# Kernel tuning notes

Hardware: AMD Instinct MI355X
Metric: run time of the kernel (lower is better)

## Reference

```python
import jax, jax.numpy as jnp
import numpy as np

N_EMBED = 384
NUM_HEADS = 6
HEAD_SIZE = 64
B, T = 128, 256


def setup_inputs() -> dict:
    key = jax.random.key(0)
    ks = jax.random.split(key, 6)
    x = jax.random.normal(ks[0], (B, T, N_EMBED), dtype=jnp.float32)
    s = 0.02
    Wq = jax.random.normal(ks[1], (NUM_HEADS, N_EMBED, HEAD_SIZE), dtype=jnp.float32) * s
    Wk = jax.random.normal(ks[2], (NUM_HEADS, N_EMBED, HEAD_SIZE), dtype=jnp.float32) * s
    Wv = jax.random.normal(ks[3], (NUM_HEADS, N_EMBED, HEAD_SIZE), dtype=jnp.float32) * s
    Wp = jax.random.normal(ks[4], (NUM_HEADS * HEAD_SIZE, N_EMBED), dtype=jnp.float32) * s
    bp = jnp.zeros((N_EMBED,), dtype=jnp.float32)
    return {"x": x, "Wq": Wq, "Wk": Wk, "Wv": Wv, "Wp": Wp, "bp": bp}


def reference(x, Wq, Wk, Wv, Wp, bp):
    # x: [B,T,C]; Wq/Wk/Wv: [H,C,hs]; Wp: [H*hs, C]
    Bx, Tx, C = x.shape
    q = jnp.einsum('btc,hcd->bhtd', x, Wq)
    k = jnp.einsum('btc,hcd->bhtd', x, Wk)
    v = jnp.einsum('btc,hcd->bhtd', x, Wv)
    scale = HEAD_SIZE ** (-0.5)
    scores = jnp.einsum('bhtd,bhsd->bhts', q, k) * scale  # [B,H,T,T]
    causal = jnp.tril(jnp.ones((Tx, Tx), dtype=bool))
    scores = jnp.where(causal, scores, -jnp.inf)
    attn = jax.nn.softmax(scores, axis=-1)
    # dropout is identity in eval mode
    out = jnp.einsum('bhts,bhsd->bhtd', attn, v)  # [B,H,T,hs]
    out = out.transpose(0, 2, 1, 3).reshape(Bx, Tx, NUM_HEADS * HEAD_SIZE)
    return out @ Wp + bp
```

## Files before the change

kernel.cpp:

```cpp
#include <hip/hip_runtime.h>
#include <hip/hip_bf16.h>

#define C_DIM 384
#define H_NUM 6
#define HS    64
#define B_DIM 128
#define T_DIM 256
#define NROWS (B_DIM * T_DIM)

typedef unsigned short u16;
typedef unsigned int u32;
typedef short bf16x8 __attribute__((ext_vector_type(8)));
typedef float floatx4 __attribute__((ext_vector_type(4)));

__device__ __forceinline__ u16 f2b(float f) {
  __hip_bfloat16 h = __float2bfloat16(f);
  u16 u;
  __builtin_memcpy(&u, &h, 2);
  return u;
}
__device__ __forceinline__ void gload_lds16(const void* g, void* lds) {
  __builtin_amdgcn_global_load_lds(
      (const __attribute__((address_space(1))) u32*)g,
      (__attribute__((address_space(3))) u32*)lds, 16, 0, 0);
}

__global__ __launch_bounds__(256) void prep_kernel(
    const float* __restrict__ x, const float* __restrict__ Wq,
    const float* __restrict__ Wk, const float* __restrict__ Wv,
    const float* __restrict__ Wp, u16* __restrict__ xb,
    u16* __restrict__ Wh, u16* __restrict__ Wpt) {
  const int bid = blockIdx.x;
  const int tid = threadIdx.x;
  if (bid < 6144) {
    const int i = bid * 256 + tid;
    const int row = (i * 8) / C_DIM;
    const int c8 = (i * 8) % C_DIM;
    const int cs = c8 ^ ((row & 7) << 3);
    const float* p = x + (size_t)row * C_DIM + cs;
    const float4 f0 = *(const float4*)p;
    const float4 f1 = *(const float4*)(p + 4);
    bf16x8 pk;
    pk[0] = (short)f2b(f0.x); pk[1] = (short)f2b(f0.y);
    pk[2] = (short)f2b(f0.z); pk[3] = (short)f2b(f0.w);
    pk[4] = (short)f2b(f1.x); pk[5] = (short)f2b(f1.y);
    pk[6] = (short)f2b(f1.z); pk[7] = (short)f2b(f1.w);
    ((bf16x8*)xb)[i] = pk;
  } else {
    const int idx = (bid - 6144) * 256 + tid;
    const int WHN = H_NUM * 192 * C_DIM;
    if (idx < WHN) {
      int h = idx / (192 * C_DIM);
      int rem = idx % (192 * C_DIM);
      int r = rem / C_DIM, c = rem % C_DIM;
      int tz = r >> 6, d = r & 63;
      const int cs = c ^ ((r & 7) << 3);
      const float* W = (tz == 0) ? Wq : (tz == 1) ? Wk : Wv;
      Wh[idx] = f2b(W[((size_t)h * C_DIM + cs) * HS + d]);
    } else {
      int j = idx - WHN;
      int n = j / C_DIM, c = j % C_DIM;
      const int cs = c ^ ((n & 7) << 3);
      Wpt[j] = f2b(Wp[cs * C_DIM + n]);
    }
  }
}

#define AS0_OFF 0
#define AS1_OFF 16384
#define BS0_OFF 32768
#define BS1_OFF 45056
#define QS_OFF  0
#define KLS_OFF 16384
#define VTS_OFF 32768
#define PLS_OFF 49152

template <bool DIAG>
__device__ __forceinline__ void attn_chunk_f(int c, int mt, int lane, int ln,
                                             int qd, const bf16x8* qf,
                                             const u16* smem, u16* Pw,
                                             floatx4* oacc, float* lsum) {
  floatx4 sacc[4];
#pragma unroll
  for (int st = 0; st < 4; ++st) {
    sacc[st] = floatx4{0.f, 0.f, 0.f, 0.f};
#pragma unroll
    for (int kc = 0; kc < 2; ++kc) {
      bf16x8 kf = *(const bf16x8*)&smem[KLS_OFF + ((c * 4 + st) * 2 + kc) * 512 +
                                        lane * 8];
      sacc[st] =
          __builtin_amdgcn_mfma_f32_16x16x32_bf16(qf[kc], kf, sacc[st], 0, 0, 0);
    }
  }
#pragma unroll
  for (int st = 0; st < 4; ++st) {
#pragma unroll
    for (int r = 0; r < 4; ++r) {
      const float sv = sacc[st][r] * 0.125f;
      float p = __expf(sv);
      if (DIAG) {
        const bool ok = (c * 64 + st * 16 + ln) <= (mt * 16 + qd * 4 + r);
        p = ok ? p : 0.f;
      }
      lsum[r] += p;
      Pw[(qd * 4 + r) * 72 + st * 16 + ln] = f2b(p);
    }
  }
#pragma unroll
  for (int kc2 = 0; kc2 < 2; ++kc2) {
    bf16x8 pf = *(const bf16x8*)&Pw[ln * 72 + kc2 * 32 + qd * 8];
#pragma unroll
    for (int dt = 0; dt < 4; ++dt) {
      bf16x8 vf = *(const bf16x8*)&smem[VTS_OFF + (dt * 16 + ln) * 256 +
                                        ((c * 64 + kc2 * 32 + qd * 8) ^
                                         ((ln & 7) << 3))];
      oacc[dt] =
          __builtin_amdgcn_mfma_f32_16x16x32_bf16(pf, vf, oacc[dt], 0, 0, 0);
    }
  }
}

__global__ __launch_bounds__(512) void qkv_attn_fused(
    const u16* __restrict__ xb, const u16* __restrict__ Wh,
    u16* __restrict__ y) {
  __shared__ __align__(16) u16 smem[58368];
  const int b = blockIdx.x;
  const int h = blockIdx.y;
  const u16* a_rows = xb + (size_t)b * 256 * C_DIM;
  const u16* wbase = Wh + (size_t)h * 192 * C_DIM;

  const int tid = threadIdx.x;
  const int lane = tid & 63;
  const int w = tid >> 6;
  const int lr = lane >> 3;
  const int lkc = (lane & 7) * 8;
  const int qd = lane >> 4;
  const int ln = lane & 15;
  const int sx = (ln & 7) << 3;
  const int wm = (w >> 1) * 64;
  const int wn = (w & 1) * 96;

  floatx4 acc[4][6];
#pragma unroll
  for (int i = 0; i < 4; ++i)
#pragma unroll
    for (int j = 0; j < 6; ++j) acc[i][j] = floatx4{0.f, 0.f, 0.f, 0.f};

#pragma unroll
  for (int s = 0; s < 4; ++s) {
    const int rbase = (s * 8 + w) * 8;
    gload_lds16(a_rows + (size_t)(rbase + lr) * C_DIM + lkc,
                smem + AS0_OFF + rbase * 64);
  }
#pragma unroll
  for (int s = 0; s < 3; ++s) {
    const int rbase = (s * 8 + w) * 8;
    gload_lds16(wbase + (size_t)(rbase + lr) * C_DIM + lkc,
                smem + BS0_OFF + rbase * 64);
  }

  for (int kb = 0; kb < 6; ++kb) {
    const int pa = (kb & 1) ? AS1_OFF : AS0_OFF;
    const int pb = (kb & 1) ? BS1_OFF : BS0_OFF;
    if (kb < 5) {
      const int qa = (kb & 1) ? AS0_OFF : AS1_OFF;
      const int qb = (kb & 1) ? BS0_OFF : BS1_OFF;
      const int k0 = (kb + 1) * 64;
#pragma unroll
      for (int s = 0; s < 4; ++s) {
        const int rbase = (s * 8 + w) * 8;
        gload_lds16(a_rows + (size_t)(rbase + lr) * C_DIM + k0 + lkc,
                    smem + qa + rbase * 64);
      }
#pragma unroll
      for (int s = 0; s < 3; ++s) {
        const int rbase = (s * 8 + w) * 8;
        gload_lds16(wbase + (size_t)(rbase + lr) * C_DIM + k0 + lkc,
                    smem + qb + rbase * 64);
      }
      asm volatile("s_waitcnt vmcnt(7)" ::: "memory");
    } else {
      asm volatile("s_waitcnt vmcnt(0)" ::: "memory");
    }
    __builtin_amdgcn_s_barrier();
    __builtin_amdgcn_sched_barrier(0);

#pragma unroll
    for (int kk = 0; kk < 2; ++kk) {
      bf16x8 af[4], bf[6];
#pragma unroll
      for (int mt = 0; mt < 4; ++mt)
        af[mt] = *(const bf16x8*)&smem[pa + (wm + mt * 16 + ln) * 64 +
                                       ((kk * 32 + qd * 8) ^ sx)];
#pragma unroll
      for (int nt = 0; nt < 6; ++nt)
        bf[nt] = *(const bf16x8*)&smem[pb + (wn + nt * 16 + ln) * 64 +
                                       ((kk * 32 + qd * 8) ^ sx)];
#pragma unroll
      for (int mt = 0; mt < 4; ++mt)
#pragma unroll
        for (int nt = 0; nt < 6; ++nt)
          acc[mt][nt] = __builtin_amdgcn_mfma_f32_16x16x32_bf16(
              af[mt], bf[nt], acc[mt][nt], 0, 0, 0);
    }
    __builtin_amdgcn_sched_barrier(0);
    __builtin_amdgcn_s_barrier();
  }

#pragma unroll
  for (int nt = 0; nt < 6; ++nt) {
    const int c0 = wn + nt * 16;
#pragma unroll
    for (int mt = 0; mt < 4; ++mt) {
#pragma unroll
      for (int r = 0; r < 4; ++r) {
        const int t = wm + mt * 16 + qd * 4 + r;
        const u16 val = f2b(acc[mt][nt][r]);
        if (c0 < 64) {
          smem[QS_OFF + t * 64 + c0 + ln] = val;
        } else if (c0 < 128) {
          const int d = c0 - 64 + ln;
          smem[KLS_OFF + ((t >> 4) << 10) + ((d >> 5) << 9) +
               (((d >> 3) & 3) << 7) + ((t & 15) << 3) + (d & 7)] = val;
        } else {
          const int dv = c0 - 128 + ln;
          smem[VTS_OFF + dv * 256 + (t ^ ((dv & 7) << 3))] = val;
        }
      }
    }
  }
  __syncthreads();

  u16* Pw = smem + PLS_OFF + w * 1152;
#pragma unroll
  for (int i = 0; i < 2; ++i) {
    const int mt = i ? (15 - w) : w;
    bf16x8 qf[2];
#pragma unroll
    for (int kc = 0; kc < 2; ++kc)
      qf[kc] = *(const bf16x8*)&smem[QS_OFF + (mt * 16 + ln) * 64 + kc * 32 +
                                     qd * 8];

    floatx4 oacc[4];
    float lsum[4];
#pragma unroll
    for (int dt = 0; dt < 4; ++dt) oacc[dt] = floatx4{0.f, 0.f, 0.f, 0.f};
#pragma unroll
    for (int r = 0; r < 4; ++r) lsum[r] = 0.f;

    const int cmax = mt >> 2;
    for (int c = 0; c < cmax; ++c)
      attn_chunk_f<false>(c, mt, lane, ln, qd, qf, smem, Pw, oacc, lsum);
    attn_chunk_f<true>(cmax, mt, lane, ln, qd, qf, smem, Pw, oacc, lsum);

#pragma unroll
    for (int off = 1; off < 16; off <<= 1)
#pragma unroll
      for (int r = 0; r < 4; ++r) lsum[r] += __shfl_xor(lsum[r], off);

#pragma unroll
    for (int r = 0; r < 4; ++r) {
      const float inv = 1.f / lsum[r];
      const int t = mt * 16 + qd * 4 + r;
      const int sy = (t & 7) << 3;
      u16* yo = y + ((size_t)b * T_DIM + t) * C_DIM + h * HS;
#pragma unroll
      for (int dt = 0; dt < 4; ++dt)
        yo[(dt * 16 + ln) ^ sy] = f2b(oacc[dt][r] * inv);
    }
  }
}

__global__ __launch_bounds__(256) void proj_gemm(
    const u16* __restrict__ yb, const u16* __restrict__ Wpt,
    const float* __restrict__ bp, float* __restrict__ out) {
  __shared__ u16 As[128 * 64];
  __shared__ u16 Bs[128 * 64];
  const int row0 = blockIdx.x * 128;
  const int n0 = blockIdx.y * 128;
  const u16* a_rows = yb + (size_t)row0 * C_DIM;
  const u16* bt_rows = Wpt + (size_t)n0 * C_DIM;

  const int tid = threadIdx.x;
  const int lane = tid & 63;
  const int w = tid >> 6;
  const int lr = lane >> 3;
  const int lkc = (lane & 7) * 8;
  const int qd = lane >> 4;
  const int ln = lane & 15;
  const int sx = (ln & 7) << 3;
  const int mw = (w >> 1) * 64;
  const int nw = (w & 1) * 64;

  floatx4 acc[4][4];
#pragma unroll
  for (int i = 0; i < 4; ++i)
#pragma unroll
    for (int j = 0; j < 4; ++j) acc[i][j] = floatx4{0.f, 0.f, 0.f, 0.f};

  for (int kb = 0; kb < C_DIM / 64; ++kb) {
    const int k0 = kb * 64;
    __syncthreads();
#pragma unroll
    for (int s = 0; s < 4; ++s) {
      const int rbase = (s * 4 + w) * 8;
      gload_lds16(a_rows + (size_t)(rbase + lr) * C_DIM + k0 + lkc,
                  As + rbase * 64);
      gload_lds16(bt_rows + (size_t)(rbase + lr) * C_DIM + k0 + lkc,
                  Bs + rbase * 64);
    }
    __syncthreads();

#pragma unroll
    for (int kk = 0; kk < 2; ++kk) {
      bf16x8 af[4], bf[4];
#pragma unroll
      for (int mt = 0; mt < 4; ++mt)
        af[mt] = *(const bf16x8*)&As[(mw + mt * 16 + ln) * 64 +
                                     ((kk * 32 + qd * 8) ^ sx)];
#pragma unroll
      for (int nt = 0; nt < 4; ++nt)
        bf[nt] = *(const bf16x8*)&Bs[(nw + nt * 16 + ln) * 64 +
                                     ((kk * 32 + qd * 8) ^ sx)];
#pragma unroll
      for (int mt = 0; mt < 4; ++mt)
#pragma unroll
        for (int nt = 0; nt < 4; ++nt)
          acc[mt][nt] = __builtin_amdgcn_mfma_f32_16x16x32_bf16(
              af[mt], bf[nt], acc[mt][nt], 0, 0, 0);
    }
  }

#pragma unroll
  for (int nt = 0; nt < 4; ++nt) {
    const int col = n0 + nw + nt * 16 + ln;
    const float bias = bp[col];
#pragma unroll
    for (int mt = 0; mt < 4; ++mt) {
#pragma unroll
      for (int r = 0; r < 4; ++r) {
        const int grow = row0 + mw + mt * 16 + qd * 4 + r;
        out[(size_t)grow * C_DIM + col] = acc[mt][nt][r] + bias;
      }
    }
  }
}

extern "C" void kernel_launch(void* const* d_in, const int* in_sizes, int n_in,
                              void* d_out, int out_size, void* d_ws, size_t ws_size,
                              hipStream_t stream) {
  const float* x  = (const float*)d_in[0];
  const float* Wq = (const float*)d_in[1];
  const float* Wk = (const float*)d_in[2];
  const float* Wv = (const float*)d_in[3];
  const float* Wp = (const float*)d_in[4];
  const float* bp = (const float*)d_in[5];
  float* out = (float*)d_out;

  const size_t n_x = (size_t)NROWS * C_DIM;

  u16* Wh  = (u16*)d_ws;
  u16* Wpt = Wh + (size_t)H_NUM * 192 * C_DIM;
  u16* xb  = Wpt + C_DIM * C_DIM;
  u16* y   = xb + n_x;

  prep_kernel<<<6144 + 2304, 256, 0, stream>>>(x, Wq, Wk, Wv, Wp, xb, Wh, Wpt);
  qkv_attn_fused<<<dim3(B_DIM, H_NUM), 512, 0, stream>>>(xb, Wh, y);
  proj_gemm<<<dim3(NROWS / 128, 3), 256, 0, stream>>>(y, Wpt, bp, out);
}
```

Baseline: 181.9 us.

## Shrink LDS footprint to raise occupancy by single-buffering and aliasing Q/V

Drops double-buffered global-to-LDS prefetch in the QKV projection loop for a single buffer with syncthreads, and reuses one LDS region first for Q (read into registers) and then for transposed V. The per-warp P scratch is halved by processing softmax/PV in 32-key halves. Together these cut shared memory from about 114KB to about 74KB and add a launch-bounds min-blocks hint, so more blocks can be resident per CU. The cost is losing load/compute overlap in the GEMM phase and adding extra barriers.

```diff
diff --git a/kernel.cpp b/kernel.cpp
--- a/kernel.cpp
+++ b/kernel.cpp
@@ -66,53 +66,52 @@
   }
 }
 
-#define AS0_OFF 0
-#define AS1_OFF 16384
-#define BS0_OFF 32768
-#define BS1_OFF 45056
-#define QS_OFF  0
-#define KLS_OFF 16384
-#define VTS_OFF 32768
-#define PLS_OFF 49152
+#define AS_OFF  0
+#define BS_OFF  16384
+#define KLS_OFF 0
+#define VQS_OFF 16384
+#define PLS_OFF 32768
 
 template <bool DIAG>
 __device__ __forceinline__ void attn_chunk_f(int c, int mt, int lane, int ln,
                                              int qd, const bf16x8* qf,
                                              const u16* smem, u16* Pw,
                                              floatx4* oacc, float* lsum) {
-  floatx4 sacc[4];
-#pragma unroll
-  for (int st = 0; st < 4; ++st) {
-    sacc[st] = floatx4{0.f, 0.f, 0.f, 0.f};
-#pragma unroll
-    for (int kc = 0; kc < 2; ++kc) {
-      bf16x8 kf = *(const bf16x8*)&smem[KLS_OFF + ((c * 4 + st) * 2 + kc) * 512 +
-                                        lane * 8];
-      sacc[st] =
-          __builtin_amdgcn_mfma_f32_16x16x32_bf16(qf[kc], kf, sacc[st], 0, 0, 0);
-    }
-  }
-#pragma unroll
-  for (int st = 0; st < 4; ++st) {
-#pragma unroll
-    for (int r = 0; r < 4; ++r) {
-      const float sv = sacc[st][r] * 0.125f;
-      float p = __expf(sv);
-      if (DIAG) {
-        const bool ok = (c * 64 + st * 16 + ln) <= (mt * 16 + qd * 4 + r);
-        p = ok ? p : 0.f;
-      }
-      lsum[r] += p;
-      Pw[(qd * 4 + r) * 72 + st * 16 + ln] = f2b(p);
-    }
-  }
-#pragma unroll
-  for (int kc2 = 0; kc2 < 2; ++kc2) {
-    bf16x8 pf = *(const bf16x8*)&Pw[ln * 72 + kc2 * 32 + qd * 8];
+#pragma unroll
+  for (int hf = 0; hf < 2; ++hf) {
+    floatx4 sacc[2];
+#pragma unroll
+    for (int s2 = 0; s2 < 2; ++s2) {
+      const int st = hf * 2 + s2;
+      sacc[s2] = floatx4{0.f, 0.f, 0.f, 0.f};
+#pragma unroll
+      for (int kc = 0; kc < 2; ++kc) {
+        bf16x8 kf = *(const bf16x8*)&smem[KLS_OFF +
+                                          ((c * 4 + st) * 2 + kc) * 512 +
+                                          lane * 8];
+        sacc[s2] = __builtin_amdgcn_mfma_f32_16x16x32_bf16(qf[kc], kf,
+                                                           sacc[s2], 0, 0, 0);
+      }
+    }
+#pragma unroll
+    for (int s2 = 0; s2 < 2; ++s2) {
+      const int st = hf * 2 + s2;
+#pragma unroll
+      for (int r = 0; r < 4; ++r) {
+        float p = __expf(sacc[s2][r] * 0.125f);
+        if (DIAG) {
+          const bool ok = (c * 64 + st * 16 + ln) <= (mt * 16 + qd * 4 + r);
+          p = ok ? p : 0.f;
+        }
+        lsum[r] += p;
+        Pw[(qd * 4 + r) * 40 + s2 * 16 + ln] = f2b(p);
+      }
+    }
+    bf16x8 pf = *(const bf16x8*)&Pw[ln * 40 + qd * 8];
 #pragma unroll
     for (int dt = 0; dt < 4; ++dt) {
-      bf16x8 vf = *(const bf16x8*)&smem[VTS_OFF + (dt * 16 + ln) * 256 +
-                                        ((c * 64 + kc2 * 32 + qd * 8) ^
+      bf16x8 vf = *(const bf16x8*)&smem[VQS_OFF + (dt * 16 + ln) * 256 +
+                                        ((c * 64 + hf * 32 + qd * 8) ^
                                          ((ln & 7) << 3))];
       oacc[dt] =
           __builtin_amdgcn_mfma_f32_16x16x32_bf16(pf, vf, oacc[dt], 0, 0, 0);
@@ -120,10 +119,10 @@
   }
 }
 
-__global__ __launch_bounds__(512) void qkv_attn_fused(
+__global__ __launch_bounds__(512, 4) void qkv_attn_fused(
     const u16* __restrict__ xb, const u16* __restrict__ Wh,
     u16* __restrict__ y) {
-  __shared__ __align__(16) u16 smem[58368];
+  __shared__ __align__(16) u16 smem[37888];
   const int b = blockIdx.x;
   const int h = blockIdx.y;
   const u16* a_rows = xb + (size_t)b * 256 * C_DIM;
@@ -146,55 +145,33 @@
 #pragma unroll
     for (int j = 0; j < 6; ++j) acc[i][j] = floatx4{0.f, 0.f, 0.f, 0.f};
 
-#pragma unroll
-  for (int s = 0; s < 4; ++s) {
-    const int rbase = (s * 8 + w) * 8;
-    gload_lds16(a_rows + (size_t)(rbase + lr) * C_DIM + lkc,
-                smem + AS0_OFF + rbase * 64);
-  }
-#pragma unroll
-  for (int s = 0; s < 3; ++s) {
-    const int rbase = (s * 8 + w) * 8;
-    gload_lds16(wbase + (size_t)(rbase + lr) * C_DIM + lkc,
-                smem + BS0_OFF + rbase * 64);
-  }
-
   for (int kb = 0; kb < 6; ++kb) {
-    const int pa = (kb & 1) ? AS1_OFF : AS0_OFF;
-    const int pb = (kb & 1) ? BS1_OFF : BS0_OFF;
-    if (kb < 5) {
-      const int qa = (kb & 1) ? AS0_OFF : AS1_OFF;
-      const int qb = (kb & 1) ? BS0_OFF : BS1_OFF;
-      const int k0 = (kb + 1) * 64;
-#pragma unroll
-      for (int s = 0; s < 4; ++s) {
-        const int rbase = (s * 8 + w) * 8;
-        gload_lds16(a_rows + (size_t)(rbase + lr) * C_DIM + k0 + lkc,
-                    smem + qa + rbase * 64);
-      }
-#pragma unroll
-      for (int s = 0; s < 3; ++s) {
-        const int rbase = (s * 8 + w) * 8;
-        gload_lds16(wbase + (size_t)(rbase + lr) * C_DIM + k0 + lkc,
-                    smem + qb + rbase * 64);
-      }
-      asm volatile("s_waitcnt vmcnt(7)" ::: "memory");
-    } else {
-      asm volatile("s_waitcnt vmcnt(0)" ::: "memory");
-    }
-    __builtin_amdgcn_s_barrier();
-    __builtin_amdgcn_sched_barrier(0);
+    const int k0 = kb * 64;
+    __syncthreads();
+#pragma unroll
+    for (int s = 0; s < 4; ++s) {
+      const int rbase = (s * 8 + w) * 8;
+      gload_lds16(a_rows + (size_t)(rbase + lr) * C_DIM + k0 + lkc,
+                  smem + AS_OFF + rbase * 64);
+    }
+#pragma unroll
+    for (int s = 0; s < 3; ++s) {
+      const int rbase = (s * 8 + w) * 8;
+      gload_lds16(wbase + (size_t)(rbase + lr) * C_DIM + k0 + lkc,
+                  smem + BS_OFF + rbase * 64);
+    }
+    __syncthreads();
 
 #pragma unroll
     for (int kk = 0; kk < 2; ++kk) {
       bf16x8 af[4], bf[6];
 #pragma unroll
       for (int mt = 0; mt < 4; ++mt)
-        af[mt] = *(const bf16x8*)&smem[pa + (wm + mt * 16 + ln) * 64 +
+        af[mt] = *(const bf16x8*)&smem[AS_OFF + (wm + mt * 16 + ln) * 64 +
                                        ((kk * 32 + qd * 8) ^ sx)];
 #pragma unroll
       for (int nt = 0; nt < 6; ++nt)
-        bf[nt] = *(const bf16x8*)&smem[pb + (wn + nt * 16 + ln) * 64 +
+        bf[nt] = *(const bf16x8*)&smem[BS_OFF + (wn + nt * 16 + ln) * 64 +
                                        ((kk * 32 + qd * 8) ^ sx)];
 #pragma unroll
       for (int mt = 0; mt < 4; ++mt)
@@ -203,43 +180,65 @@
           acc[mt][nt] = __builtin_amdgcn_mfma_f32_16x16x32_bf16(
               af[mt], bf[nt], acc[mt][nt], 0, 0, 0);
     }
-    __builtin_amdgcn_sched_barrier(0);
-    __builtin_amdgcn_s_barrier();
-  }
+  }
+  __syncthreads();
 
 #pragma unroll
   for (int nt = 0; nt < 6; ++nt) {
     const int c0 = wn + nt * 16;
-#pragma unroll
-    for (int mt = 0; mt < 4; ++mt) {
-#pragma unroll
-      for (int r = 0; r < 4; ++r) {
-        const int t = wm + mt * 16 + qd * 4 + r;
-        const u16 val = f2b(acc[mt][nt][r]);
-        if (c0 < 64) {
-          smem[QS_OFF + t * 64 + c0 + ln] = val;
-        } else if (c0 < 128) {
-          const int d = c0 - 64 + ln;
-          smem[KLS_OFF + ((t >> 4) << 10) + ((d >> 5) << 9) +
-               (((d >> 3) & 3) << 7) + ((t & 15) << 3) + (d & 7)] = val;
-        } else {
-          const int dv = c0 - 128 + ln;
-          smem[VTS_OFF + dv * 256 + (t ^ ((dv & 7) << 3))] = val;
+    if (c0 < 128) {
+#pragma unroll
+      for (int mt = 0; mt < 4; ++mt) {
+#pragma unroll
+        for (int r = 0; r < 4; ++r) {
+          const int t = wm + mt * 16 + qd * 4 + r;
+          const u16 val = f2b(acc[mt][nt][r]);
+          if (c0 < 64) {
+            smem[VQS_OFF + t * 64 + ((c0 + ln) ^ ((t & 7) << 3))] = val;
+          } else {
+            const int d = c0 - 64 + ln;
+            smem[KLS_OFF + ((t >> 4) << 10) + ((d >> 5) << 9) +
+                 (((d >> 3) & 3) << 7) + ((t & 15) << 3) + (d & 7)] = val;
+          }
         }
       }
     }
   }
   __syncthreads();
 
-  u16* Pw = smem + PLS_OFF + w * 1152;
+  bf16x8 qf2[2][2];
 #pragma unroll
   for (int i = 0; i < 2; ++i) {
     const int mt = i ? (15 - w) : w;
-    bf16x8 qf[2];
 #pragma unroll
     for (int kc = 0; kc < 2; ++kc)
-      qf[kc] = *(const bf16x8*)&smem[QS_OFF + (mt * 16 + ln) * 64 + kc * 32 +
-                                     qd * 8];
+      qf2[i][kc] = *(const bf16x8*)&smem[VQS_OFF + (mt * 16 + ln) * 64 +
+                                         ((kc * 32 + qd * 8) ^ sx)];
+  }
+  __syncthreads();
+
+#pragma unroll
+  for (int nt = 2; nt < 6; ++nt) {
+    const int c0 = wn + nt * 16;
+    if (c0 >= 128) {
+#pragma unroll
+      for (int mt = 0; mt < 4; ++mt) {
+#pragma unroll
+        for (int r = 0; r < 4; ++r) {
+          const int t = wm + mt * 16 + qd * 4 + r;
+          const int dv = c0 - 128 + ln;
+          smem[VQS_OFF + dv * 256 + (t ^ ((dv & 7) << 3))] =
+              f2b(acc[mt][nt][r]);
+        }
+      }
+    }
+  }
+  __syncthreads();
+
+  u16* Pw = smem + PLS_OFF + w * 640;
+#pragma unroll
+  for (int i = 0; i < 2; ++i) {
+    const int mt = i ? (15 - w) : w;
 
     floatx4 oacc[4];
     float lsum[4];
@@ -250,8 +249,8 @@
 
     const int cmax = mt >> 2;
     for (int c = 0; c < cmax; ++c)
-      attn_chunk_f<false>(c, mt, lane, ln, qd, qf, smem, Pw, oacc, lsum);
-    attn_chunk_f<true>(cmax, mt, lane, ln, qd, qf, smem, Pw, oacc, lsum);
+      attn_chunk_f<false>(c, mt, lane, ln, qd, qf2[i], smem, Pw, oacc, lsum);
+    attn_chunk_f<true>(cmax, mt, lane, ln, qd, qf2[i], smem, Pw, oacc, lsum);
 
 #pragma unroll
     for (int off = 1; off < 16; off <<= 1)
```

Measured after the change: 293.7 us. +61.5%, slower.

## Double-buffer LDS tiles in projection GEMM to overlap loads with MFMA

Applied to the files above, without the earlier changes.

The output projection GEMM now keeps two LDS buffers for the A and B tiles and prefetches the next k-block through direct global-to-LDS loads while MFMAs run on the current one. Explicit vmcnt waits and raw barriers replace the two __syncthreads per iteration. The intent is to hide global load latency in the projection kernel. In exchange, LDS use per block doubles to 64KB, which may cut occupancy, and the hand-written waitcnt values must match the number of loads in flight.

```diff
diff --git a/kernel.cpp b/kernel.cpp
--- a/kernel.cpp
+++ b/kernel.cpp
@@ -271,11 +271,15 @@
   }
 }
 
+#define PAS0 0
+#define PAS1 8192
+#define PBS0 16384
+#define PBS1 24576
+
 __global__ __launch_bounds__(256) void proj_gemm(
     const u16* __restrict__ yb, const u16* __restrict__ Wpt,
     const float* __restrict__ bp, float* __restrict__ out) {
-  __shared__ u16 As[128 * 64];
-  __shared__ u16 Bs[128 * 64];
+  __shared__ __align__(16) u16 smem[32768];
   const int row0 = blockIdx.x * 128;
   const int n0 = blockIdx.y * 128;
   const u16* a_rows = yb + (size_t)row0 * C_DIM;
@@ -298,30 +302,48 @@
 #pragma unroll
     for (int j = 0; j < 4; ++j) acc[i][j] = floatx4{0.f, 0.f, 0.f, 0.f};
 
-  for (int kb = 0; kb < C_DIM / 64; ++kb) {
-    const int k0 = kb * 64;
-    __syncthreads();
-#pragma unroll
-    for (int s = 0; s < 4; ++s) {
-      const int rbase = (s * 4 + w) * 8;
-      gload_lds16(a_rows + (size_t)(rbase + lr) * C_DIM + k0 + lkc,
-                  As + rbase * 64);
-      gload_lds16(bt_rows + (size_t)(rbase + lr) * C_DIM + k0 + lkc,
-                  Bs + rbase * 64);
-    }
-    __syncthreads();
+#pragma unroll
+  for (int s = 0; s < 4; ++s) {
+    const int rbase = (s * 4 + w) * 8;
+    gload_lds16(a_rows + (size_t)(rbase + lr) * C_DIM + lkc,
+                smem + PAS0 + rbase * 64);
+    gload_lds16(bt_rows + (size_t)(rbase + lr) * C_DIM + lkc,
+                smem + PBS0 + rbase * 64);
+  }
+
+  for (int kb = 0; kb < 6; ++kb) {
+    const int pa = (kb & 1) ? PAS1 : PAS0;
+    const int pb = (kb & 1) ? PBS1 : PBS0;
+    if (kb < 5) {
+      const int qa = (kb & 1) ? PAS0 : PAS1;
+      const int qb = (kb & 1) ? PBS0 : PBS1;
+      const int k0 = (kb + 1) * 64;
+#pragma unroll
+      for (int s = 0; s < 4; ++s) {
+        const int rbase = (s * 4 + w) * 8;
+        gload_lds16(a_rows + (size_t)(rbase + lr) * C_DIM + k0 + lkc,
+                    smem + qa + rbase * 64);
+        gload_lds16(bt_rows + (size_t)(rbase + lr) * C_DIM + k0 + lkc,
+                    smem + qb + rbase * 64);
+      }
+      asm volatile("s_waitcnt vmcnt(8)" ::: "memory");
+    } else {
+      asm volatile("s_waitcnt vmcnt(0)" ::: "memory");
+    }
+    __builtin_amdgcn_s_barrier();
+    __builtin_amdgcn_sched_barrier(0);
 
 #pragma unroll
     for (int kk = 0; kk < 2; ++kk) {
       bf16x8 af[4], bf[4];
 #pragma unroll
       for (int mt = 0; mt < 4; ++mt)
-        af[mt] = *(const bf16x8*)&As[(mw + mt * 16 + ln) * 64 +
-                                     ((kk * 32 + qd * 8) ^ sx)];
+        af[mt] = *(const bf16x8*)&smem[pa + (mw + mt * 16 + ln) * 64 +
+                                       ((kk * 32 + qd * 8) ^ sx)];
 #pragma unroll
       for (int nt = 0; nt < 4; ++nt)
-        bf[nt] = *(const bf16x8*)&Bs[(nw + nt * 16 + ln) * 64 +
-                                     ((kk * 32 + qd * 8) ^ sx)];
+        bf[nt] = *(const bf16x8*)&smem[pb + (nw + nt * 16 + ln) * 64 +
+                                       ((kk * 32 + qd * 8) ^ sx)];
 #pragma unroll
       for (int mt = 0; mt < 4; ++mt)
 #pragma unroll
@@ -329,6 +351,8 @@
           acc[mt][nt] = __builtin_amdgcn_mfma_f32_16x16x32_bf16(
               af[mt], bf[nt], acc[mt][nt], 0, 0, 0);
     }
+    __builtin_amdgcn_sched_barrier(0);
+    __builtin_amdgcn_s_barrier();
   }
 
 #pragma unroll
```

Result: no change. 182.1 us (+0.1%).
